# Optimization experiments

Hardware: AMD Instinct MI355X
Metric: run time of the kernel (lower is better)

The kernel has to match this reference:

```python
import jax, jax.numpy as jnp
import numpy as np

ITERS = 3
K = 64
C = 256


def setup_inputs() -> dict:
    key = jax.random.key(0)
    ks = jax.random.split(key, 6)
    N, H, W = 2, 60, 60
    cnn_feature = jax.random.normal(ks[0], (N, C, H, W), dtype=jnp.float32)
    points = jax.random.normal(ks[1], (N, 3, H, W), dtype=jnp.float32)
    # torch Linear params: weight (out, in), bias (out,)
    s1 = 1.0 / np.sqrt(C)
    s2 = 1.0 / np.sqrt(2 * C)
    mlp_w = jax.random.uniform(ks[2], (C, C), jnp.float32, -s1, s1)
    mlp_b = jax.random.uniform(ks[3], (C,), jnp.float32, -s1, s1)
    rnn_w = jax.random.uniform(ks[4], (C, 2 * C), jnp.float32, -s2, s2)
    rnn_b = jax.random.uniform(ks[5], (C,), jnp.float32, -s2, s2)
    return {"cnn_feature": cnn_feature, "points": points, "mlp_w": mlp_w,
            "mlp_b": mlp_b, "rnn_w": rnn_w, "rnn_b": rnn_b}


def reference(cnn_feature, points, mlp_w, mlp_b, rnn_w, rnn_b):
    N, Cc, H, W = cnn_feature.shape
    HW = H * W
    pts = points.reshape(N, 3, HW).transpose(0, 2, 1)  # (N, HW, 3)
    # pairwise Euclidean distances via Gram matrix
    r = jnp.einsum('nid,njd->nij', pts, pts)           # (N, HW, HW)
    sq = jnp.einsum('nid,nid->ni', pts, pts)           # (N, HW)
    D = jnp.sqrt(jnp.maximum(sq[:, :, None] + sq[:, None, :] - 2.0 * r, 0.0))
    _, idx = jax.lax.top_k(-D, K)                      # (N, HW, K) smallest distances

    h = cnn_feature.transpose(0, 2, 3, 1).reshape(N, HW, Cc)  # (N, HW, C)
    bidx = jnp.arange(N)[:, None, None]
    for _ in range(ITERS):
        nb = h[bidx, idx]                              # (N, HW, K, C) gather
        nb = jax.nn.relu(jnp.einsum('nskc,dc->nskd', nb, mlp_w) + mlp_b)
        message = nb.mean(axis=2)                      # (N, HW, C)
        nh = jnp.concatenate([h, message], axis=-1)    # (N, HW, 2C)
        h = jax.nn.relu(jnp.einsum('nsc,dc->nsd', nh, rnn_w) + rnn_b)
    h = h.reshape(N, H, W, Cc).transpose(0, 3, 1, 2)   # (N, C, H, W)
    return jnp.concatenate([cnn_feature, h], axis=1)   # (N, 2C, H, W)
```

## Files before the change

kernel.cpp:

```cpp
#include <hip/hip_runtime.h>
#include <stdint.h>

typedef unsigned int uint;
typedef unsigned long long ull;

#define HW 3600
#define NBATCH 2
#define CDIM 256
#define KNN 64
#define M_REAL 7200
#define PADM 7232
#define QPB 8

#define TKB 900
#define IHB 904
#define SUB 64

using short8  = __attribute__((ext_vector_type(8))) short;
using floatx4 = __attribute__((ext_vector_type(4))) float;

__device__ inline unsigned short f2bf(float f) {
    uint u = __float_as_uint(f);
    uint r = u + 0x7FFFu + ((u >> 16) & 1u);
    return (unsigned short)(r >> 16);
}
__device__ inline float bf2f(unsigned short b) {
    return __uint_as_float(((uint)b) << 16);
}

__device__ inline void wave_select(uint* hist, uint* s_bin, uint* s_want,
                                   int lane, uint want) {
    uint h0 = hist[4 * lane + 0], h1 = hist[4 * lane + 1];
    uint h2 = hist[4 * lane + 2], h3 = hist[4 * lane + 3];
    hist[4 * lane + 0] = 0; hist[4 * lane + 1] = 0;
    hist[4 * lane + 2] = 0; hist[4 * lane + 3] = 0;
    uint c4 = h0 + h1 + h2 + h3;
    uint v = c4;
    #pragma unroll
    for (int off = 1; off < 64; off <<= 1) {
        uint o = __shfl_up(v, off, 64);
        if (lane >= off) v += o;
    }
    uint below = v - c4;
    if (below < want && want <= v) {
        uint b = 4 * lane, c = below;
        if (c + h0 < want) { c += h0; b = 4 * lane + 1;
            if (c + h1 < want) { c += h1; b = 4 * lane + 2;
                if (c + h2 < want) { c += h2; b = 4 * lane + 3; } } }
        *s_bin = b;
        *s_want = want - c;
    }
}

union MegaSmem {
    struct {
        float4 pts[HW];
        uint hist[QPB][256];
        uint s_bin[QPB], s_want[QPB], s_cnt[QPB];
    } tk;
    struct { float tile[2][32][33]; } ih;
};

__global__ __launch_bounds__(512) void mega_kernel(
    const float* __restrict__ points, int* __restrict__ idx_out,
    const float* __restrict__ cnn, unsigned short* __restrict__ NH,
    float* __restrict__ out,
    const float* __restrict__ mw, const float* __restrict__ rw,
    unsigned short* __restrict__ mo, unsigned short* __restrict__ ro) {
    __shared__ MegaSmem sm;
    const int blk = blockIdx.x;

    if (blk >= TKB + IHB) {
        int i0 = (blk - TKB - IHB) * 2048 + threadIdx.x * 4;
        float4 v = *(const float4*)&rw[i0];
        uint2 p;
        p.x = (uint)f2bf(v.x) | ((uint)f2bf(v.y) << 16);
        p.y = (uint)f2bf(v.z) | ((uint)f2bf(v.w) << 16);
        *(uint2*)&ro[i0] = p;
        if (i0 < 65536) {
            float4 m = *(const float4*)&mw[i0];
            p.x = (uint)f2bf(m.x) | ((uint)f2bf(m.y) << 16);
            p.y = (uint)f2bf(m.z) | ((uint)f2bf(m.w) << 16);
            *(uint2*)&mo[i0] = p;
        }
        return;
    }

    if (blk >= TKB) {
        const int b = blk - TKB;
        const int n = b / 452;
        const int r = b - n * 452;
        const int hw0 = (r % 113) * 32;
        const int c0 = (r / 113) * 64 + ((threadIdx.x >> 8) << 5);
        const int t8 = threadIdx.x & 255;
        const int tx = t8 & 31;
        const int ty = t8 >> 5;
        float (*tile)[33] = sm.ih.tile[threadIdx.x >> 8];
        const float* __restrict__ src = cnn + (size_t)n * CDIM * HW;
        #pragma unroll
        for (int rr = 0; rr < 4; ++rr) {
            int cc = ty + rr * 8;
            int hw = hw0 + tx;
            if (hw < HW) {
                float v = src[(size_t)(c0 + cc) * HW + hw];
                tile[cc][tx] = v;
                out[(size_t)n * (2 * CDIM * HW) + (size_t)(c0 + cc) * HW + hw] = v;
            }
        }
        __syncthreads();
        #pragma unroll
        for (int rr = 0; rr < 4; ++rr) {
            int hh = ty + rr * 8;
            int hw = hw0 + hh;
            if (hw < HW)
                NH[(size_t)(n * HW + hw) * 512 + c0 + tx] = f2bf(tile[tx][hh]);
        }
        return;
    }

    const int wv = threadIdx.x >> 6;
    const int lane = threadIdx.x & 63;
    const int q = blk * QPB + wv;
    const int n = (blk * QPB) / HW;
    const int i = q - n * HW;

    const float* __restrict__ px = points + (size_t)n * 3 * HW;
    const float* __restrict__ py = px + HW;
    const float* __restrict__ pz = py + HW;

    for (int j = threadIdx.x; j < HW; j += 512)
        sm.tk.pts[j] = make_float4(px[j], py[j], pz[j], 0.0f);
    sm.tk.hist[wv][4 * lane + 0] = 0; sm.tk.hist[wv][4 * lane + 1] = 0;
    sm.tk.hist[wv][4 * lane + 2] = 0; sm.tk.hist[wv][4 * lane + 3] = 0;
    if (lane == 0) sm.tk.s_cnt[wv] = 0;
    __syncthreads();

    float4 pq = sm.tk.pts[i];
    const float xi = pq.x, yi = pq.y, zi = pq.z;
    const float sqi = xi * xi + yi * yi + zi * zi;

    uint qp[29];
    #pragma unroll
    for (int s = 0; s < 57; ++s) {
        int j = (s << 6) + lane;
        uint q16 = 0xFFFFu;
        if (j < HW) {
            float4 p = sm.tk.pts[j];
            float d2 = fmaxf(sqi + (p.x * p.x + p.y * p.y + p.z * p.z)
                             - 2.0f * (xi * p.x + yi * p.y + zi * p.z), 0.0f);
            q16 = (uint)fminf(d2 * 1024.0f, 65535.0f);
        }
        if (s & 1) qp[s >> 1] |= q16 << 16; else qp[s >> 1] = q16;
    }
    #define Q16(s) ((qp[(s) >> 1] >> (((s) & 1) << 4)) & 0xFFFFu)

    #pragma unroll
    for (int s = 0; s < 57; ++s) {
        int j = (s << 6) + lane;
        if (j < HW) atomicAdd(&sm.tk.hist[wv][Q16(s) >> 8], 1u);
    }
    __syncthreads();
    wave_select(&sm.tk.hist[wv][0], &sm.tk.s_bin[wv], &sm.tk.s_want[wv], lane, KNN);
    __syncthreads();
    const uint qT8 = sm.tk.s_bin[wv];
    const uint want2 = sm.tk.s_want[wv];
    __syncthreads();

    #pragma unroll
    for (int s = 0; s < 57; ++s) {
        int j = (s << 6) + lane;
        uint k = Q16(s);
        if (j < HW && (k >> 8) == qT8)
            atomicAdd(&sm.tk.hist[wv][k & 255u], 1u);
    }
    __syncthreads();
    wave_select(&sm.tk.hist[wv][0], &sm.tk.s_bin[wv], &sm.tk.s_want[wv], lane, want2);
    __syncthreads();
    const uint qT16 = (qT8 << 8) | sm.tk.s_bin[wv];
    const uint want3 = sm.tk.s_want[wv];

    #pragma unroll
    for (int s = 0; s < 57; ++s) {
        if (Q16(s) < qT16) {
            uint pos = atomicAdd(&sm.tk.s_cnt[wv], 1u);
            if (pos < KNN) idx_out[(size_t)q * KNN + pos] = (s << 6) + lane;
        }
    }

    ull cand[4] = {~0ULL, ~0ULL, ~0ULL, ~0ULL};
    int ncand = 0;
    #pragma unroll
    for (int s = 0; s < 57; ++s) {
        int j = (s << 6) + lane;
        if (j < HW && Q16(s) == qT16) {
            float4 p = sm.tk.pts[j];
            float d2 = fmaxf(sqi + (p.x * p.x + p.y * p.y + p.z * p.z)
                             - 2.0f * (xi * p.x + yi * p.y + zi * p.z), 0.0f);
            ull key = ((ull)__float_as_uint(d2) << 32) | (uint)j;
            if      (ncand == 0) cand[0] = key;
            else if (ncand == 1) cand[1] = key;
            else if (ncand == 2) cand[2] = key;
            else if (ncand == 3) cand[3] = key;
            ++ncand;
        }
    }
    const int base = KNN - (int)want3;
    if (__ballot(ncand > 4) == 0ULL) {
        for (int r = 0; r < (int)want3; ++r) {
            ull best = cand[0] < cand[1] ? cand[0] : cand[1];
            ull b23  = cand[2] < cand[3] ? cand[2] : cand[3];
            best = best < b23 ? best : b23;
            #pragma unroll
            for (int off = 1; off < 64; off <<= 1) {
                ull o = __shfl_xor(best, off, 64);
                if (o < best) best = o;
            }
            if (lane == 0) idx_out[(size_t)q * KNN + base + r] = (int)(uint)best;
            #pragma unroll
            for (int c = 0; c < 4; ++c)
                if (cand[c] == best) cand[c] = ~0ULL;
        }
    } else {
        ull used = 0ULL;
        for (int r = 0; r < (int)want3; ++r) {
            ull best = ~0ULL;
            #pragma unroll
            for (int s = 0; s < 57; ++s) {
                int j = (s << 6) + lane;
                if (j < HW && Q16(s) == qT16 && !((used >> s) & 1ULL)) {
                    float4 p = sm.tk.pts[j];
                    float d2 = fmaxf(sqi + (p.x * p.x + p.y * p.y + p.z * p.z)
                                     - 2.0f * (xi * p.x + yi * p.y + zi * p.z), 0.0f);
                    ull key = ((ull)__float_as_uint(d2) << 32) | (uint)j;
                    if (key < best) best = key;
                }
            }
            #pragma unroll
            for (int off = 1; off < 64; off <<= 1) {
                ull o = __shfl_xor(best, off, 64);
                if (o < best) best = o;
            }
            uint jw = (uint)best;
            if (lane == 0) idx_out[(size_t)q * KNN + base + r] = (int)jw;
            if ((int)(jw & 63u) == lane) used |= 1ULL << (jw >> 6);
        }
    }
    #undef Q16
}

#define LDKP 264
__global__ __launch_bounds__(256) void gemm_mfma(
    const unsigned short* __restrict__ A, int lda,
    const unsigned short* __restrict__ W, int ldw,
    const float* __restrict__ bias,
    unsigned short* __restrict__ Cb, int ldc,
    float* __restrict__ outp, int mode, int Kk) {
    __shared__ __align__(16) unsigned short As[64 * LDKP];
    __shared__ __align__(16) unsigned short Bs[64 * LDKP];
    const int m0 = blockIdx.x * 64;
    const int n0 = blockIdx.y * 64;
    const int tid = threadIdx.x;
    const int lane = tid & 63;
    const int w = tid >> 6;
    const int wm = (w & 1) * 32;
    const int wn = (w >> 1) * 32;
    const int l15 = lane & 15;
    const int qd = lane >> 4;

    floatx4 acc[2][2];
    #pragma unroll
    for (int a = 0; a < 2; ++a)
        #pragma unroll
        for (int b = 0; b < 2; ++b)
            acc[a][b] = (floatx4){0.f, 0.f, 0.f, 0.f};

    const int srow = tid >> 5;
    const int scol = (tid & 31) * 8;

    for (int k0 = 0; k0 < Kk; k0 += 256) {
        if (k0) __syncthreads();
        #pragma unroll
        for (int r8 = 0; r8 < 8; ++r8) {
            int row = r8 * 8 + srow;
            *(float4*)&As[row * LDKP + scol] =
                *(const float4*)&A[(size_t)(m0 + row) * lda + k0 + scol];
            *(float4*)&Bs[row * LDKP + scol] =
                *(const float4*)&W[(size_t)(n0 + row) * ldw + k0 + scol];
        }
        __syncthreads();
        #pragma unroll
        for (int ks = 0; ks < 256; ks += 32) {
            short8 a0 = *(const short8*)&As[(wm + l15) * LDKP + ks + qd * 8];
            short8 a1 = *(const short8*)&As[(wm + 16 + l15) * LDKP + ks + qd * 8];
            short8 b0 = *(const short8*)&Bs[(wn + l15) * LDKP + ks + qd * 8];
            short8 b1 = *(const short8*)&Bs[(wn + 16 + l15) * LDKP + ks + qd * 8];
            acc[0][0] = __builtin_amdgcn_mfma_f32_16x16x32_bf16(a0, b0, acc[0][0], 0, 0, 0);
            acc[0][1] = __builtin_amdgcn_mfma_f32_16x16x32_bf16(a0, b1, acc[0][1], 0, 0, 0);
            acc[1][0] = __builtin_amdgcn_mfma_f32_16x16x32_bf16(a1, b0, acc[1][0], 0, 0, 0);
            acc[1][1] = __builtin_amdgcn_mfma_f32_16x16x32_bf16(a1, b1, acc[1][1], 0, 0, 0);
        }
    }

    #pragma unroll
    for (int in = 0; in < 2; ++in) {
        int col = n0 + wn + in * 16 + l15;
        float bv = bias[col];
        #pragma unroll
        for (int im = 0; im < 2; ++im) {
            int mb = m0 + wm + im * 16 + qd * 4;
            if (mode == 0) {
                #pragma unroll
                for (int r = 0; r < 4; ++r)
                    Cb[(size_t)(mb + r) * ldc + col] =
                        f2bf(fmaxf(acc[im][in][r] + bv, 0.0f));
            } else if (mb < M_REAL) {
                int nb = mb / HW;
                int hw = mb - nb * HW;
                float4 o;
                o.x = fmaxf(acc[im][in][0] + bv, 0.0f);
                o.y = fmaxf(acc[im][in][1] + bv, 0.0f);
                o.z = fmaxf(acc[im][in][2] + bv, 0.0f);
                o.w = fmaxf(acc[im][in][3] + bv, 0.0f);
                *(float4*)&outp[(size_t)nb * (2 * CDIM * HW)
                                + (size_t)(CDIM + col) * HW + hw] = o;
            }
        }
    }
}

__global__ __launch_bounds__(256) void gather_mean(const unsigned short* __restrict__ T,
                                                   const int* __restrict__ idx,
                                                   unsigned short* __restrict__ NH) {
    const int q = blockIdx.x * 4 + (threadIdx.x >> 6);
    const int lane = threadIdx.x & 63;
    const int n = q / HW;
    const int half = lane >> 5;
    const int c8 = (lane & 31) * 8;

    const int nbrL = idx[(size_t)q * KNN + lane];
    float acc[8] = {0, 0, 0, 0, 0, 0, 0, 0};
    #pragma unroll 4
    for (int it = 0; it < 32; ++it) {
        int k = 2 * it + half;
        int j = __shfl(nbrL, k, 64);
        j = min(max(j, 0), HW - 1);
        int r = n * HW + j;
        uint4 v = *(const uint4*)&T[(size_t)r * CDIM + c8];
        acc[0] += bf2f((unsigned short)(v.x & 0xFFFFu));
        acc[1] += bf2f((unsigned short)(v.x >> 16));
        acc[2] += bf2f((unsigned short)(v.y & 0xFFFFu));
        acc[3] += bf2f((unsigned short)(v.y >> 16));
        acc[4] += bf2f((unsigned short)(v.z & 0xFFFFu));
        acc[5] += bf2f((unsigned short)(v.z >> 16));
        acc[6] += bf2f((unsigned short)(v.w & 0xFFFFu));
        acc[7] += bf2f((unsigned short)(v.w >> 16));
    }
    #pragma unroll
    for (int c = 0; c < 8; ++c) acc[c] += __shfl_xor(acc[c], 32, 64);
    if (half == 0) {
        uint4 o;
        o.x = (uint)f2bf(acc[0] * (1.0f / KNN)) | ((uint)f2bf(acc[1] * (1.0f / KNN)) << 16);
        o.y = (uint)f2bf(acc[2] * (1.0f / KNN)) | ((uint)f2bf(acc[3] * (1.0f / KNN)) << 16);
        o.z = (uint)f2bf(acc[4] * (1.0f / KNN)) | ((uint)f2bf(acc[5] * (1.0f / KNN)) << 16);
        o.w = (uint)f2bf(acc[6] * (1.0f / KNN)) | ((uint)f2bf(acc[7] * (1.0f / KNN)) << 16);
        *(uint4*)&NH[(size_t)q * 512 + CDIM + c8] = o;
    }
}

extern "C" void kernel_launch(void* const* d_in, const int* in_sizes, int n_in,
                              void* d_out, int out_size, void* d_ws, size_t ws_size,
                              hipStream_t stream) {
    const float* cnn   = (const float*)d_in[0];
    const float* pts   = (const float*)d_in[1];
    const float* mlp_w = (const float*)d_in[2];
    const float* mlp_b = (const float*)d_in[3];
    const float* rnn_w = (const float*)d_in[4];
    const float* rnn_b = (const float*)d_in[5];
    float* out = (float*)d_out;

    unsigned short* NHa    = (unsigned short*)d_ws;
    unsigned short* NHb    = NHa + (size_t)PADM * 512;
    unsigned short* Tb     = NHb + (size_t)PADM * 512;
    unsigned short* mlpw_b = Tb + (size_t)PADM * CDIM;
    unsigned short* rnnw_b = mlpw_b + 65536;
    int*            idx    = (int*)(rnnw_b + 131072);

    mega_kernel<<<TKB + IHB + SUB, 512, 0, stream>>>(
        pts, idx, cnn, NHa, out, mlp_w, rnn_w, mlpw_b, rnnw_b);

    unsigned short* cur = NHa;
    unsigned short* nxt = NHb;
    for (int it = 0; it < 3; ++it) {
        gemm_mfma<<<dim3(PADM / 64, CDIM / 64), 256, 0, stream>>>(
            cur, 512, mlpw_b, CDIM, mlp_b, Tb, CDIM, nullptr, 0, CDIM);
        gather_mean<<<M_REAL / 4, 256, 0, stream>>>(Tb, idx, cur);
        if (it < 2) {
            gemm_mfma<<<dim3(PADM / 64, CDIM / 64), 256, 0, stream>>>(
                cur, 512, rnnw_b, 512, rnn_b, nxt, 512, nullptr, 0, 512);
            unsigned short* tmp = cur; cur = nxt; nxt = tmp;
        } else {
            gemm_mfma<<<dim3(PADM / 64, CDIM / 64), 256, 0, stream>>>(
                cur, 512, rnnw_b, 512, rnn_b, nullptr, 0, out, 1, 512);
        }
    }
}
```

Baseline: 206.8 us.

## Fuse first MLP GEMM into mega kernel, interleave blocks, use wave-local LDS fences

Moves the first iteration's MLP GEMM into the mega kernel as extra blocks that read fp32 cnn features and fp32 MLP weights directly, converting to bf16 in LDS, so one standalone GEMM launch disappears. Top-k blocks are interleaved with the transpose and GEMM blocks so their work overlaps across CUs. Block-wide __syncthreads in the per-wave histogram select are replaced by s_waitcnt fences, since each wave uses only its own histogram. This adds LDS pressure in the union and relies on wave-local ordering being sufficient for correctness.

```diff
diff --git a/kernel.cpp b/kernel.cpp
--- a/kernel.cpp
+++ b/kernel.cpp
@@ -13,8 +13,12 @@
 #define QPB 8
 
 #define TKB 900
+#define TK1 512
+#define TKI 388
 #define IHB 904
+#define GEB 452
 #define SUB 64
+#define MEGA_BLOCKS (TKB + IHB + GEB + SUB)
 
 using short8  = __attribute__((ext_vector_type(8))) short;
 using floatx4 = __attribute__((ext_vector_type(4))) float;
@@ -52,6 +56,9 @@
     }
 }
 
+#define WAVE_LDS_FENCE() asm volatile("s_waitcnt lgkmcnt(0)" ::: "memory")
+
+#define LDKP 264
 union MegaSmem {
     struct {
         float4 pts[HW];
@@ -59,6 +66,7 @@
         uint s_bin[QPB], s_want[QPB], s_cnt[QPB];
     } tk;
     struct { float tile[2][32][33]; } ih;
+    struct { unsigned short As[64 * LDKP]; unsigned short Bs[64 * LDKP]; } ge;
 };
 
 __global__ __launch_bounds__(512) void mega_kernel(
@@ -66,12 +74,131 @@
     const float* __restrict__ cnn, unsigned short* __restrict__ NH,
     float* __restrict__ out,
     const float* __restrict__ mw, const float* __restrict__ rw,
-    unsigned short* __restrict__ mo, unsigned short* __restrict__ ro) {
+    unsigned short* __restrict__ mo, unsigned short* __restrict__ ro,
+    const float* __restrict__ mlp_bias, unsigned short* __restrict__ Tb) {
     __shared__ MegaSmem sm;
     const int blk = blockIdx.x;
 
-    if (blk >= TKB + IHB) {
-        int i0 = (blk - TKB - IHB) * 2048 + threadIdx.x * 4;
+    int tkb = -1, oth = -1;
+    if (blk < TK1) tkb = blk;
+    else if (blk < TK1 + 2 * TKI) {
+        int t = blk - TK1;
+        if ((t & 1) == 0) tkb = TK1 + (t >> 1);
+        else oth = t >> 1;
+    } else oth = TKI + (blk - (TK1 + 2 * TKI));
+
+    if (tkb < 0) {
+        if (oth < IHB) {
+            const int b = oth;
+            const int n = b / 452;
+            const int r = b - n * 452;
+            const int hw0 = (r % 113) * 32;
+            const int c0 = (r / 113) * 64 + ((threadIdx.x >> 8) << 5);
+            const int t8 = threadIdx.x & 255;
+            const int tx = t8 & 31;
+            const int ty = t8 >> 5;
+            float (*tile)[33] = sm.ih.tile[threadIdx.x >> 8];
+            const float* __restrict__ src = cnn + (size_t)n * CDIM * HW;
+            #pragma unroll
+            for (int rr = 0; rr < 4; ++rr) {
+                int cc = ty + rr * 8;
+                int hw = hw0 + tx;
+                if (hw < HW) {
+                    float v = src[(size_t)(c0 + cc) * HW + hw];
+                    tile[cc][tx] = v;
+                    out[(size_t)n * (2 * CDIM * HW) + (size_t)(c0 + cc) * HW + hw] = v;
+                }
+            }
+            __syncthreads();
+            #pragma unroll
+            for (int rr = 0; rr < 4; ++rr) {
+                int hh = ty + rr * 8;
+                int hw = hw0 + hh;
+                if (hw < HW)
+                    NH[(size_t)(n * HW + hw) * 512 + c0 + tx] = f2bf(tile[tx][hh]);
+            }
+            return;
+        }
+        if (oth < IHB + GEB) {
+            const int g = oth - IHB;
+            const int m0 = (g % 113) * 64;
+            const int n0 = (g / 113) * 64;
+            const int tid = threadIdx.x;
+
+            const bool fast = (m0 + 64 <= HW) || (m0 >= HW && m0 + 64 <= M_REAL);
+            if (fast) {
+                const int nn = m0 >= HW;
+                const float* __restrict__ base =
+                    cnn + (size_t)nn * CDIM * HW + (m0 - nn * HW);
+                #pragma unroll
+                for (int i = 0; i < 8; ++i) {
+                    int L = i * 512 + tid;
+                    int c = L >> 4, seg = L & 15;
+                    float4 v = *(const float4*)&base[(size_t)c * HW + seg * 4];
+                    sm.ge.As[(seg * 4 + 0) * LDKP + c] = f2bf(v.x);
+                    sm.ge.As[(seg * 4 + 1) * LDKP + c] = f2bf(v.y);
+                    sm.ge.As[(seg * 4 + 2) * LDKP + c] = f2bf(v.z);
+                    sm.ge.As[(seg * 4 + 3) * LDKP + c] = f2bf(v.w);
+                }
+            } else {
+                #pragma unroll
+                for (int i = 0; i < 8; ++i) {
+                    int L = i * 512 + tid;
+                    int c = L >> 4, seg = L & 15;
+                    #pragma unroll
+                    for (int k = 0; k < 4; ++k) {
+                        int m = m0 + seg * 4 + k;
+                        float v = 0.0f;
+                        if (m < M_REAL) {
+                            int nn = m >= HW;
+                            v = cnn[(size_t)nn * CDIM * HW + (size_t)c * HW
+                                    + (m - nn * HW)];
+                        }
+                        sm.ge.As[(seg * 4 + k) * LDKP + c] = f2bf(v);
+                    }
+                }
+            }
+            #pragma unroll
+            for (int i = 0; i < 8; ++i) {
+                int L = i * 512 + tid;
+                int row = L >> 6, k4 = (L & 63) * 4;
+                float4 v = *(const float4*)&mw[(size_t)(n0 + row) * CDIM + k4];
+                uint2 p;
+                p.x = (uint)f2bf(v.x) | ((uint)f2bf(v.y) << 16);
+                p.y = (uint)f2bf(v.z) | ((uint)f2bf(v.w) << 16);
+                *(uint2*)&sm.ge.Bs[row * LDKP + k4] = p;
+            }
+            __syncthreads();
+
+            const int w = tid >> 6;
+            const int lane = tid & 63;
+            const int l15 = lane & 15;
+            const int qd = lane >> 4;
+            const int wm = (w & 1) * 32;
+            const int wn = (w >> 1) * 16;
+            floatx4 acc0 = (floatx4){0.f, 0.f, 0.f, 0.f};
+            floatx4 acc1 = (floatx4){0.f, 0.f, 0.f, 0.f};
+            #pragma unroll
+            for (int ks = 0; ks < 256; ks += 32) {
+                short8 a0 = *(const short8*)&sm.ge.As[(wm + l15) * LDKP + ks + qd * 8];
+                short8 a1 = *(const short8*)&sm.ge.As[(wm + 16 + l15) * LDKP + ks + qd * 8];
+                short8 b0 = *(const short8*)&sm.ge.Bs[(wn + l15) * LDKP + ks + qd * 8];
+                acc0 = __builtin_amdgcn_mfma_f32_16x16x32_bf16(a0, b0, acc0, 0, 0, 0);
+                acc1 = __builtin_amdgcn_mfma_f32_16x16x32_bf16(a1, b0, acc1, 0, 0, 0);
+            }
+            const int col = n0 + wn + l15;
+            const float bv = mlp_bias[col];
+            #pragma unroll
+            for (int im = 0; im < 2; ++im) {
+                int mb = m0 + wm + im * 16 + qd * 4;
+                floatx4 a = im ? acc1 : acc0;
+                #pragma unroll
+                for (int r = 0; r < 4; ++r)
+                    Tb[(size_t)(mb + r) * CDIM + col] = f2bf(fmaxf(a[r] + bv, 0.0f));
+            }
+            return;
+        }
+        int i0 = (oth - IHB - GEB) * 2048 + threadIdx.x * 4;
         float4 v = *(const float4*)&rw[i0];
         uint2 p;
         p.x = (uint)f2bf(v.x) | ((uint)f2bf(v.y) << 16);
@@ -86,42 +213,10 @@
         return;
     }
 
-    if (blk >= TKB) {
-        const int b = blk - TKB;
-        const int n = b / 452;
-        const int r = b - n * 452;
-        const int hw0 = (r % 113) * 32;
-        const int c0 = (r / 113) * 64 + ((threadIdx.x >> 8) << 5);
-        const int t8 = threadIdx.x & 255;
-        const int tx = t8 & 31;
-        const int ty = t8 >> 5;
-        float (*tile)[33] = sm.ih.tile[threadIdx.x >> 8];
-        const float* __restrict__ src = cnn + (size_t)n * CDIM * HW;
-        #pragma unroll
-        for (int rr = 0; rr < 4; ++rr) {
-            int cc = ty + rr * 8;
-            int hw = hw0 + tx;
-            if (hw < HW) {
-                float v = src[(size_t)(c0 + cc) * HW + hw];
-                tile[cc][tx] = v;
-                out[(size_t)n * (2 * CDIM * HW) + (size_t)(c0 + cc) * HW + hw] = v;
-            }
-        }
-        __syncthreads();
-        #pragma unroll
-        for (int rr = 0; rr < 4; ++rr) {
-            int hh = ty + rr * 8;
-            int hw = hw0 + hh;
-            if (hw < HW)
-                NH[(size_t)(n * HW + hw) * 512 + c0 + tx] = f2bf(tile[tx][hh]);
-        }
-        return;
-    }
-
     const int wv = threadIdx.x >> 6;
     const int lane = threadIdx.x & 63;
-    const int q = blk * QPB + wv;
-    const int n = (blk * QPB) / HW;
+    const int q = tkb * QPB + wv;
+    const int n = (tkb * QPB) / HW;
     const int i = q - n * HW;
 
     const float* __restrict__ px = points + (size_t)n * 3 * HW;
@@ -159,12 +254,11 @@
         int j = (s << 6) + lane;
         if (j < HW) atomicAdd(&sm.tk.hist[wv][Q16(s) >> 8], 1u);
     }
-    __syncthreads();
+    WAVE_LDS_FENCE();
     wave_select(&sm.tk.hist[wv][0], &sm.tk.s_bin[wv], &sm.tk.s_want[wv], lane, KNN);
-    __syncthreads();
+    WAVE_LDS_FENCE();
     const uint qT8 = sm.tk.s_bin[wv];
     const uint want2 = sm.tk.s_want[wv];
-    __syncthreads();
 
     #pragma unroll
     for (int s = 0; s < 57; ++s) {
@@ -173,9 +267,9 @@
         if (j < HW && (k >> 8) == qT8)
             atomicAdd(&sm.tk.hist[wv][k & 255u], 1u);
     }
-    __syncthreads();
+    WAVE_LDS_FENCE();
     wave_select(&sm.tk.hist[wv][0], &sm.tk.s_bin[wv], &sm.tk.s_want[wv], lane, want2);
-    __syncthreads();
+    WAVE_LDS_FENCE();
     const uint qT16 = (qT8 << 8) | sm.tk.s_bin[wv];
     const uint want3 = sm.tk.s_want[wv];
 
@@ -248,7 +342,6 @@
     #undef Q16
 }
 
-#define LDKP 264
 __global__ __launch_bounds__(256) void gemm_mfma(
     const unsigned short* __restrict__ A, int lda,
     const unsigned short* __restrict__ W, int ldw,
@@ -385,19 +478,19 @@
     unsigned short* rnnw_b = mlpw_b + 65536;
     int*            idx    = (int*)(rnnw_b + 131072);
 
-    mega_kernel<<<TKB + IHB + SUB, 512, 0, stream>>>(
-        pts, idx, cnn, NHa, out, mlp_w, rnn_w, mlpw_b, rnnw_b);
+    mega_kernel<<<MEGA_BLOCKS, 512, 0, stream>>>(
+        pts, idx, cnn, NHa, out, mlp_w, rnn_w, mlpw_b, rnnw_b, mlp_b, Tb);
 
     unsigned short* cur = NHa;
     unsigned short* nxt = NHb;
     for (int it = 0; it < 3; ++it) {
-        gemm_mfma<<<dim3(PADM / 64, CDIM / 64), 256, 0, stream>>>(
-            cur, 512, mlpw_b, CDIM, mlp_b, Tb, CDIM, nullptr, 0, CDIM);
         gather_mean<<<M_REAL / 4, 256, 0, stream>>>(Tb, idx, cur);
         if (it < 2) {
             gemm_mfma<<<dim3(PADM / 64, CDIM / 64), 256, 0, stream>>>(
                 cur, 512, rnnw_b, 512, rnn_b, nxt, 512, nullptr, 0, 512);
             unsigned short* tmp = cur; cur = nxt; nxt = tmp;
+            gemm_mfma<<<dim3(PADM / 64, CDIM / 64), 256, 0, stream>>>(
+                cur, 512, mlpw_b, CDIM, mlp_b, Tb, CDIM, nullptr, 0, CDIM);
         } else {
             gemm_mfma<<<dim3(PADM / 64, CDIM / 64), 256, 0, stream>>>(
                 cur, 512, rnnw_b, 512, rnn_b, nullptr, 0, out, 1, 512);
```

Result: slower. 231.0 us (+11.7%).

## Split RNN GEMM so its hidden-state half runs alongside the MLP GEMM

Applied to the files above, without the earlier changes.

The RNN linear layer is split into two halves over K. The half that multiplies the previous hidden state now runs in the same launch as the MLP GEMM, and its fp32 partial result goes to a scratch buffer P. A second kernel multiplies the message half, adds P and applies the ReLU, writing the new hidden state in place, which removes the ping-pong NH buffer. This moves GEMM work off the critical path after gather_mean and halves the shared-memory tile per block, at the cost of an extra fp32 round trip through P. In the top-k section, block-wide barriers around the per-wave histogram selection are replaced with wave-local LDS waitcnt fences.

```diff
diff --git a/kernel.cpp b/kernel.cpp
--- a/kernel.cpp
+++ b/kernel.cpp
@@ -5,7 +5,6 @@
 typedef unsigned long long ull;
 
 #define HW 3600
-#define NBATCH 2
 #define CDIM 256
 #define KNN 64
 #define M_REAL 7200
@@ -16,6 +15,8 @@
 #define IHB 904
 #define SUB 64
 
+#define LDB2 136
+
 using short8  = __attribute__((ext_vector_type(8))) short;
 using floatx4 = __attribute__((ext_vector_type(4))) float;
 
@@ -27,6 +28,8 @@
 __device__ inline float bf2f(unsigned short b) {
     return __uint_as_float(((uint)b) << 16);
 }
+
+#define WAVE_LDS_FENCE() asm volatile("s_waitcnt lgkmcnt(0)" ::: "memory")
 
 __device__ inline void wave_select(uint* hist, uint* s_bin, uint* s_want,
                                    int lane, uint want) {
@@ -159,12 +162,11 @@
         int j = (s << 6) + lane;
         if (j < HW) atomicAdd(&sm.tk.hist[wv][Q16(s) >> 8], 1u);
     }
-    __syncthreads();
+    WAVE_LDS_FENCE();
     wave_select(&sm.tk.hist[wv][0], &sm.tk.s_bin[wv], &sm.tk.s_want[wv], lane, KNN);
-    __syncthreads();
+    WAVE_LDS_FENCE();
     const uint qT8 = sm.tk.s_bin[wv];
     const uint want2 = sm.tk.s_want[wv];
-    __syncthreads();
 
     #pragma unroll
     for (int s = 0; s < 57; ++s) {
@@ -173,9 +175,9 @@
         if (j < HW && (k >> 8) == qT8)
             atomicAdd(&sm.tk.hist[wv][k & 255u], 1u);
     }
-    __syncthreads();
+    WAVE_LDS_FENCE();
     wave_select(&sm.tk.hist[wv][0], &sm.tk.s_bin[wv], &sm.tk.s_want[wv], lane, want2);
-    __syncthreads();
+    WAVE_LDS_FENCE();
     const uint qT16 = (qT8 << 8) | sm.tk.s_bin[wv];
     const uint want3 = sm.tk.s_want[wv];
 
@@ -248,17 +250,25 @@
     #undef Q16
 }
 
-#define LDKP 264
-__global__ __launch_bounds__(256) void gemm_mfma(
-    const unsigned short* __restrict__ A, int lda,
-    const unsigned short* __restrict__ W, int ldw,
-    const float* __restrict__ bias,
-    unsigned short* __restrict__ Cb, int ldc,
-    float* __restrict__ outp, int mode, int Kk) {
-    __shared__ __align__(16) unsigned short As[64 * LDKP];
-    __shared__ __align__(16) unsigned short Bs[64 * LDKP];
-    const int m0 = blockIdx.x * 64;
-    const int n0 = blockIdx.y * 64;
+
+__global__ __launch_bounds__(256) void gemm_dual(
+    const unsigned short* __restrict__ NH,
+    const unsigned short* __restrict__ mwb,
+    const float* __restrict__ mbias,
+    const unsigned short* __restrict__ rwb,
+    const float* __restrict__ rbias,
+    unsigned short* __restrict__ Tb,
+    float* __restrict__ P) {
+    __shared__ __align__(16) unsigned short As[64 * LDB2];
+    __shared__ __align__(16) unsigned short Bs[64 * LDB2];
+    const int v = blockIdx.x;
+    const bool is_mlp = v < 452;
+    const int g = is_mlp ? v : v - 452;
+    const int m0 = (g % 113) * 64;
+    const int n0 = (g / 113) * 64;
+    const unsigned short* __restrict__ W = is_mlp ? mwb : rwb;
+    const int ldw = is_mlp ? 256 : 512;
+
     const int tid = threadIdx.x;
     const int lane = tid & 63;
     const int w = tid >> 6;
@@ -274,26 +284,26 @@
         for (int b = 0; b < 2; ++b)
             acc[a][b] = (floatx4){0.f, 0.f, 0.f, 0.f};
 
-    const int srow = tid >> 5;
-    const int scol = (tid & 31) * 8;
-
-    for (int k0 = 0; k0 < Kk; k0 += 256) {
-        if (k0) __syncthreads();
-        #pragma unroll
-        for (int r8 = 0; r8 < 8; ++r8) {
-            int row = r8 * 8 + srow;
-            *(float4*)&As[row * LDKP + scol] =
-                *(const float4*)&A[(size_t)(m0 + row) * lda + k0 + scol];
-            *(float4*)&Bs[row * LDKP + scol] =
-                *(const float4*)&W[(size_t)(n0 + row) * ldw + k0 + scol];
+    const int srow = tid >> 4;
+    const int scol = (tid & 15) * 8;
+
+    for (int kc = 0; kc < 256; kc += 128) {
+        if (kc) __syncthreads();
+        #pragma unroll
+        for (int r4 = 0; r4 < 4; ++r4) {
+            int row = r4 * 16 + srow;
+            *(float4*)&As[row * LDB2 + scol] =
+                *(const float4*)&NH[(size_t)(m0 + row) * 512 + kc + scol];
+            *(float4*)&Bs[row * LDB2 + scol] =
+                *(const float4*)&W[(size_t)(n0 + row) * ldw + kc + scol];
         }
         __syncthreads();
         #pragma unroll
-        for (int ks = 0; ks < 256; ks += 32) {
-            short8 a0 = *(const short8*)&As[(wm + l15) * LDKP + ks + qd * 8];
-            short8 a1 = *(const short8*)&As[(wm + 16 + l15) * LDKP + ks + qd * 8];
-            short8 b0 = *(const short8*)&Bs[(wn + l15) * LDKP + ks + qd * 8];
-            short8 b1 = *(const short8*)&Bs[(wn + 16 + l15) * LDKP + ks + qd * 8];
+        for (int ks = 0; ks < 128; ks += 32) {
+            short8 a0 = *(const short8*)&As[(wm + l15) * LDB2 + ks + qd * 8];
+            short8 a1 = *(const short8*)&As[(wm + 16 + l15) * LDB2 + ks + qd * 8];
+            short8 b0 = *(const short8*)&Bs[(wn + l15) * LDB2 + ks + qd * 8];
+            short8 b1 = *(const short8*)&Bs[(wn + 16 + l15) * LDB2 + ks + qd * 8];
             acc[0][0] = __builtin_amdgcn_mfma_f32_16x16x32_bf16(a0, b0, acc[0][0], 0, 0, 0);
             acc[0][1] = __builtin_amdgcn_mfma_f32_16x16x32_bf16(a0, b1, acc[0][1], 0, 0, 0);
             acc[1][0] = __builtin_amdgcn_mfma_f32_16x16x32_bf16(a1, b0, acc[1][0], 0, 0, 0);
@@ -304,23 +314,97 @@
     #pragma unroll
     for (int in = 0; in < 2; ++in) {
         int col = n0 + wn + in * 16 + l15;
-        float bv = bias[col];
+        float bv = is_mlp ? mbias[col] : rbias[col];
+        #pragma unroll
+        for (int im = 0; im < 2; ++im) {
+            int mb = m0 + wm + im * 16 + qd * 4;
+            if (is_mlp) {
+                #pragma unroll
+                for (int r = 0; r < 4; ++r)
+                    Tb[(size_t)(mb + r) * CDIM + col] =
+                        f2bf(fmaxf(acc[im][in][r] + bv, 0.0f));
+            } else {
+                #pragma unroll
+                for (int r = 0; r < 4; ++r)
+                    P[(size_t)(mb + r) * CDIM + col] = acc[im][in][r] + bv;
+            }
+        }
+    }
+}
+
+__global__ __launch_bounds__(256) void gemm_rnn2(
+    const unsigned short* __restrict__ NH,
+    const unsigned short* __restrict__ rwb,
+    const float* __restrict__ P,
+    unsigned short* __restrict__ Cb,
+    float* __restrict__ outp, int mode) {
+    __shared__ __align__(16) unsigned short As[64 * LDB2];
+    __shared__ __align__(16) unsigned short Bs[64 * LDB2];
+    const int m0 = (blockIdx.x % 113) * 64;
+    const int n0 = (blockIdx.x / 113) * 64;
+
+    const int tid = threadIdx.x;
+    const int lane = tid & 63;
+    const int w = tid >> 6;
+    const int wm = (w & 1) * 32;
+    const int wn = (w >> 1) * 32;
+    const int l15 = lane & 15;
+    const int qd = lane >> 4;
+
+    floatx4 acc[2][2];
+    #pragma unroll
+    for (int a = 0; a < 2; ++a)
+        #pragma unroll
+        for (int b = 0; b < 2; ++b)
+            acc[a][b] = (floatx4){0.f, 0.f, 0.f, 0.f};
+
+    const int srow = tid >> 4;
+    const int scol = (tid & 15) * 8;
+
+    for (int kc = 0; kc < 256; kc += 128) {
+        if (kc) __syncthreads();
+        #pragma unroll
+        for (int r4 = 0; r4 < 4; ++r4) {
+            int row = r4 * 16 + srow;
+            *(float4*)&As[row * LDB2 + scol] =
+                *(const float4*)&NH[(size_t)(m0 + row) * 512 + 256 + kc + scol];
+            *(float4*)&Bs[row * LDB2 + scol] =
+                *(const float4*)&rwb[(size_t)(n0 + row) * 512 + 256 + kc + scol];
+        }
+        __syncthreads();
+        #pragma unroll
+        for (int ks = 0; ks < 128; ks += 32) {
+            short8 a0 = *(const short8*)&As[(wm + l15) * LDB2 + ks + qd * 8];
+            short8 a1 = *(const short8*)&As[(wm + 16 + l15) * LDB2 + ks + qd * 8];
+            short8 b0 = *(const short8*)&Bs[(wn + l15) * LDB2 + ks + qd * 8];
+            short8 b1 = *(const short8*)&Bs[(wn + 16 + l15) * LDB2 + ks + qd * 8];
+            acc[0][0] = __builtin_amdgcn_mfma_f32_16x16x32_bf16(a0, b0, acc[0][0], 0, 0, 0);
+            acc[0][1] = __builtin_amdgcn_mfma_f32_16x16x32_bf16(a0, b1, acc[0][1], 0, 0, 0);
+            acc[1][0] = __builtin_amdgcn_mfma_f32_16x16x32_bf16(a1, b0, acc[1][0], 0, 0, 0);
+            acc[1][1] = __builtin_amdgcn_mfma_f32_16x16x32_bf16(a1, b1, acc[1][1], 0, 0, 0);
+        }
+    }
+
+    #pragma unroll
+    for (int in = 0; in < 2; ++in) {
+        int col = n0 + wn + in * 16 + l15;
         #pragma unroll
         for (int im = 0; im < 2; ++im) {
             int mb = m0 + wm + im * 16 + qd * 4;
             if (mode == 0) {
                 #pragma unroll
-                for (int r = 0; r < 4; ++r)
-                    Cb[(size_t)(mb + r) * ldc + col] =
-                        f2bf(fmaxf(acc[im][in][r] + bv, 0.0f));
+                for (int r = 0; r < 4; ++r) {
+                    float o = fmaxf(acc[im][in][r] + P[(size_t)(mb + r) * CDIM + col], 0.0f);
+                    Cb[(size_t)(mb + r) * 512 + col] = f2bf(o);
+                }
             } else if (mb < M_REAL) {
                 int nb = mb / HW;
                 int hw = mb - nb * HW;
                 float4 o;
-                o.x = fmaxf(acc[im][in][0] + bv, 0.0f);
-                o.y = fmaxf(acc[im][in][1] + bv, 0.0f);
-                o.z = fmaxf(acc[im][in][2] + bv, 0.0f);
-                o.w = fmaxf(acc[im][in][3] + bv, 0.0f);
+                o.x = fmaxf(acc[im][in][0] + P[(size_t)(mb + 0) * CDIM + col], 0.0f);
+                o.y = fmaxf(acc[im][in][1] + P[(size_t)(mb + 1) * CDIM + col], 0.0f);
+                o.z = fmaxf(acc[im][in][2] + P[(size_t)(mb + 2) * CDIM + col], 0.0f);
+                o.w = fmaxf(acc[im][in][3] + P[(size_t)(mb + 3) * CDIM + col], 0.0f);
                 *(float4*)&outp[(size_t)nb * (2 * CDIM * HW)
                                 + (size_t)(CDIM + col) * HW + hw] = o;
             }
@@ -379,8 +463,8 @@
     float* out = (float*)d_out;
 
     unsigned short* NHa    = (unsigned short*)d_ws;
-    unsigned short* NHb    = NHa + (size_t)PADM * 512;
-    unsigned short* Tb     = NHb + (size_t)PADM * 512;
+    float*          P      = (float*)(NHa + (size_t)PADM * 512);
+    unsigned short* Tb     = (unsigned short*)(P + (size_t)PADM * CDIM);
     unsigned short* mlpw_b = Tb + (size_t)PADM * CDIM;
     unsigned short* rnnw_b = mlpw_b + 65536;
     int*            idx    = (int*)(rnnw_b + 131072);
@@ -388,19 +472,16 @@
     mega_kernel<<<TKB + IHB + SUB, 512, 0, stream>>>(
         pts, idx, cnn, NHa, out, mlp_w, rnn_w, mlpw_b, rnnw_b);
 
-    unsigned short* cur = NHa;
-    unsigned short* nxt = NHb;
     for (int it = 0; it < 3; ++it) {
-        gemm_mfma<<<dim3(PADM / 64, CDIM / 64), 256, 0, stream>>>(
-            cur, 512, mlpw_b, CDIM, mlp_b, Tb, CDIM, nullptr, 0, CDIM);
-        gather_mean<<<M_REAL / 4, 256, 0, stream>>>(Tb, idx, cur);
+        gemm_dual<<<904, 256, 0, stream>>>(
+            NHa, mlpw_b, mlp_b, rnnw_b, rnn_b, Tb, P);
+        gather_mean<<<M_REAL / 4, 256, 0, stream>>>(Tb, idx, NHa);
         if (it < 2) {
-            gemm_mfma<<<dim3(PADM / 64, CDIM / 64), 256, 0, stream>>>(
-                cur, 512, rnnw_b, 512, rnn_b, nxt, 512, nullptr, 0, 512);
-            unsigned short* tmp = cur; cur = nxt; nxt = tmp;
+            gemm_rnn2<<<452, 256, 0, stream>>>(
+                NHa, rnnw_b, P, NHa, nullptr, 0);
         } else {
-            gemm_mfma<<<dim3(PADM / 64, CDIM / 64), 256, 0, stream>>>(
-                cur, 512, rnnw_b, 512, rnn_b, nullptr, 0, out, 1, 512);
-        }
-    }
-}
+            gemm_rnn2<<<452, 256, 0, stream>>>(
+                NHa, rnnw_b, P, nullptr, out, 1);
+        }
+    }
+}
```

New measurement: 209.9 us. No clear change (+1.5%).
